# Performance work log

Measured on AMD Instinct MI355X. Metric: run time of the kernel, lower is better.

The kernel has to match this reference:

```python
import jax, jax.numpy as jnp
import numpy as np

N = 1048576   # total nodes
E = 8388608   # total edges
IN = 5        # in_channels
H = 32        # hid_channels
G = 16384     # num graphs
C = 10        # num_classes
L = 2         # conv_unit
EPS = 1e-5


def setup_inputs() -> dict:
    key = jax.random.key(0)
    ks = jax.random.split(key, 16)
    x = jax.random.normal(ks[0], (N, IN), dtype=jnp.float32)
    edge_index = jax.random.randint(ks[1], (2, E), 0, N, dtype=jnp.int64)
    edge_attr = jax.random.uniform(ks[2], (E, 1), dtype=jnp.float32)
    batch = jnp.sort(jax.random.randint(ks[3], (N,), 0, G, dtype=jnp.int64))
    s_in = 1.0 / np.sqrt(IN)
    s_h = 1.0 / np.sqrt(H)
    s_2h = 1.0 / np.sqrt(2 * H)
    W_emb = jax.random.normal(ks[4], (H, IN), dtype=jnp.float32) * s_in
    b_emb = jnp.zeros((H,), dtype=jnp.float32)
    W_rel = jax.random.normal(ks[5], (L, H, H), dtype=jnp.float32) * s_h
    b_rel = jnp.zeros((L, H), dtype=jnp.float32)
    W_root = jax.random.normal(ks[6], (L, H, H), dtype=jnp.float32) * s_h
    bn_gamma = jnp.ones((L, H), dtype=jnp.float32)
    bn_beta = jnp.zeros((L, H), dtype=jnp.float32)
    W1 = jax.random.normal(ks[7], (2 * H, H), dtype=jnp.float32) * s_h
    b1 = jnp.zeros((2 * H,), dtype=jnp.float32)
    W2 = jax.random.normal(ks[8], (C, 2 * H), dtype=jnp.float32) * s_2h
    b2 = jnp.zeros((C,), dtype=jnp.float32)
    return {
        "x": x, "edge_index": edge_index, "edge_attr": edge_attr, "batch": batch,
        "W_emb": W_emb, "b_emb": b_emb, "W_rel": W_rel, "b_rel": b_rel,
        "W_root": W_root, "bn_gamma": bn_gamma, "bn_beta": bn_beta,
        "W1": W1, "b1": b1, "W2": W2, "b2": b2,
    }


def _graph_conv(x, src, dst, ew, Wrel, brel, Wroot):
    # PyG GraphConv: lin_rel(scatter_add(ew * x[src] -> dst)) + lin_root(x)
    msg = x[src] * ew[:, None]                              # [E, H]
    agg = jax.ops.segment_sum(msg, dst, num_segments=N)     # [N, H]
    return agg @ Wrel.T + brel + x @ Wroot.T


def _batch_norm(x, gamma, beta):
    mean = jnp.mean(x, axis=0)
    var = jnp.mean(jnp.square(x - mean), axis=0)  # biased, as torch training BN
    return (x - mean) * jax.lax.rsqrt(var + EPS) * gamma + beta


def reference(x, edge_index, edge_attr, batch, W_emb, b_emb, W_rel, b_rel,
              W_root, bn_gamma, bn_beta, W1, b1, W2, b2):
    src, dst = edge_index[0], edge_index[1]
    ew = edge_attr.reshape(-1)
    h = x @ W_emb.T + b_emb                                  # node_emb
    for i in range(L):
        h = _graph_conv(h, src, dst, ew, W_rel[i], b_rel[i], W_root[i])
        h = jax.nn.relu(_batch_norm(h, bn_gamma[i], bn_beta[i]))
    graph_x = jax.ops.segment_max(h, batch, num_segments=G)  # global_max_pool
    hidden = jax.nn.relu(graph_x @ W1.T + b1)
    return hidden @ W2.T + b2                                # [G, C]
```

## Files before the change

### kernel.cpp

```cpp
#include <hip/hip_runtime.h>
#include <hip/hip_fp16.h>

#define NN 1048576
#define NE 8388608
#define NG 16384
#define NBUCK 256
#define BSH 12
#define EPB (NE / 256)

typedef _Float16 half8 __attribute__((ext_vector_type(8)));
typedef float f32x16 __attribute__((ext_vector_type(16)));

__global__ __launch_bounds__(256) void k_embed(const float* __restrict__ x,
    const float* __restrict__ W, const float* __restrict__ b, __half* __restrict__ h) {
  __shared__ float sW[160];
  __shared__ float sb[32];
  int t = threadIdx.x;
  if (t < 160) sW[t] = W[t];
  if (t < 32) sb[t] = b[t];
  __syncthreads();
  int idx = blockIdx.x * 256 + t;
  int c = idx & 31, n = idx >> 5;
  const float* xr = x + n * 5;
  float acc = sb[c];
#pragma unroll
  for (int k = 0; k < 5; ++k) acc = fmaf(xr[k], sW[c * 5 + k], acc);
  h[idx] = __float2half(acc);
}

__global__ __launch_bounds__(256) void k_pcnt(const int* __restrict__ dst, int* __restrict__ hist) {
  __shared__ int lh[NBUCK];
  int t = threadIdx.x;
  lh[t] = 0;
  __syncthreads();
  int base = blockIdx.x * EPB;
  for (int e = base + t; e < base + EPB; e += 256)
    atomicAdd(&lh[dst[e] >> BSH], 1);
  __syncthreads();
  hist[t * 256 + blockIdx.x] = lh[t];
}

__global__ __launch_bounds__(256) void k_scanA(int* __restrict__ hist, int* __restrict__ tot) {
  __shared__ int s2[256];
  int b = blockIdx.x, t = threadIdx.x;
  int v = hist[b * 256 + t];
  s2[t] = v; __syncthreads();
  for (int st = 1; st < 256; st <<= 1) {
    int a = (t >= st) ? s2[t - st] : 0; __syncthreads(); s2[t] += a; __syncthreads();
  }
  hist[b * 256 + t] = s2[t] - v;
  if (t == 255) tot[b] = s2[255];
}

__global__ __launch_bounds__(256) void k_scanB(const int* __restrict__ tot, int* __restrict__ gbase) {
  __shared__ int s2[256];
  int t = threadIdx.x;
  int c = tot[t];
  s2[t] = c; __syncthreads();
  for (int st = 1; st < 256; st <<= 1) {
    int a = (t >= st) ? s2[t - st] : 0; __syncthreads(); s2[t] += a; __syncthreads();
  }
  gbase[t] = s2[t] - c;
  if (t == 255) gbase[256] = s2[255];
}

__global__ __launch_bounds__(256) void k_part(const int* __restrict__ ei, const float* __restrict__ ew,
                                              const int* __restrict__ hist, const int* __restrict__ gbase,
                                              uint2* __restrict__ bsw) {
  __shared__ int cur[NBUCK];
  int t = threadIdx.x, blk = blockIdx.x;
  cur[t] = gbase[t] + hist[t * 256 + blk];
  __syncthreads();
  int base = blk * EPB;
  for (int e = base + t; e < base + EPB; e += 256) {
    int src = ei[e];
    int d   = ei[NE + e];
    unsigned wb = __float_as_uint(ew[e]);
    int b = d >> BSH;
    int pos = atomicAdd(&cur[b], 1);
    bsw[pos] = make_uint2(((unsigned)src << 12) | (unsigned)(d & 4095), wb);
  }
}

__global__ __launch_bounds__(256) void k_fillD(const int* __restrict__ gbase, const uint2* __restrict__ bsw,
                                               int* __restrict__ rowptr, uint2* __restrict__ colw) {
  __shared__ int loc[4096];
  __shared__ int s2[256];
  int t = threadIdx.x, b = blockIdx.x;
  int beg = gbase[b], end = gbase[b + 1], gb = beg;
  int node_base = b << BSH;
#pragma unroll
  for (int j = 0; j < 16; ++j) loc[t * 16 + j] = 0;
  __syncthreads();
  for (int i = beg + t; i < end; i += 256) atomicAdd(&loc[bsw[i].x & 4095], 1);
  __syncthreads();
  int v[16]; int tsum = 0;
#pragma unroll
  for (int j = 0; j < 16; ++j) { v[j] = loc[t * 16 + j]; tsum += v[j]; }
  s2[t] = tsum; __syncthreads();
  for (int st = 1; st < 256; st <<= 1) {
    int a = (t >= st) ? s2[t - st] : 0; __syncthreads(); s2[t] += a; __syncthreads();
  }
  int run = s2[t] - tsum;
#pragma unroll
  for (int j = 0; j < 16; ++j) {
    loc[t * 16 + j] = run;
    rowptr[node_base + t * 16 + j] = gb + run;
    run += v[j];
  }
  if (b == NBUCK - 1 && t == 255) rowptr[NN] = NE;
  __syncthreads();
  for (int i = beg + t; i < end; i += 256) {
    uint2 r = bsw[i];
    int p = atomicAdd(&loc[r.x & 4095], 1);
    colw[gb + p] = make_uint2(r.x >> 12, r.y);
  }
}

__global__ __launch_bounds__(256) void k_gbound(const int* __restrict__ batch, int* __restrict__ gptr) {
  int n = blockIdx.x * 256 + threadIdx.x;
  int b = batch[n];
  int prev = (n == 0) ? -1 : batch[n - 1];
  for (int g = prev + 1; g <= b; ++g) gptr[g] = n;
  if (n == NN - 1) {
    for (int g = b + 1; g <= NG; ++g) gptr[g] = NN;
  }
}

template <int FUSE_BN>
__global__ __launch_bounds__(256) void k_agglin(
    const int* __restrict__ rowptr, const uint2* __restrict__ colw,
    const __half* __restrict__ hIn, const float* __restrict__ bnss,
    const float* __restrict__ Wrel, const float* __restrict__ brel,
    const float* __restrict__ Wroot, __half* __restrict__ hPre,
    double* __restrict__ stats) {
  __shared__ __half sA[4][1024];
  __shared__ uint2 sE[256];
  __shared__ float sBn[64];
  __shared__ double rS[256], rQ[256];
  int t = threadIdx.x;
  int wv = t >> 6, lane = t & 63;
  int c = lane & 31, hi = lane >> 5, grp = t >> 5;
  int slot = (lane >> 4) & 1, cl = lane & 15;
  char* myA = (char*)sA[wv];

  if (FUSE_BN && t < 64) sBn[t] = bnss[t];
  __syncthreads();

  float bs0x = 0.f, bs0y = 0.f, bs1x = 0.f, bs1y = 0.f;
  if constexpr (FUSE_BN) {
    bs0x = bnss[2 * cl];      bs0y = bnss[2 * cl + 1];
    bs1x = bnss[32 + 2 * cl]; bs1y = bnss[32 + 2 * cl + 1];
  }

  half8 bfr[4];
#pragma unroll
  for (int m = 0; m < 4; ++m)
#pragma unroll
    for (int j = 0; j < 8; ++j) {
      int k = 16 * m + hi * 8 + j;
      float w = (k < 32) ? Wrel[c * 32 + k] : Wroot[c * 32 + (k - 32)];
      bfr[m][j] = (_Float16)w;
    }
  float bias = brel[c];
  double aS = 0.0, aQ = 0.0;

  for (int tile = blockIdx.x * 4 + wv; tile < NN / 32; tile += gridDim.x * 4) {
    int nbase = tile * 32;
    for (int r = 0; r < 16; ++r) {
      int node = 2 * r + hi;
      int n = nbase + node;
      int r0 = rowptr[n], r1 = rowptr[n + 1];
      float2 acc = make_float2(0.f, 0.f);
      for (int j = r0; j < r1; j += 32) {
        int m_ = r1 - j; if (m_ > 32) m_ = 32;
        uint2 cw = make_uint2(0u, 0u);
        if (c < m_) cw = colw[j + c];
        sE[t] = cw;
        int mm = (m_ + 7) & ~7;
        for (int i = 0; i < mm; i += 8) {
#pragma unroll
          for (int k = 0; k < 4; ++k) {
            uint2 e = sE[grp * 32 + i + 2 * k + slot];
            __half2 hv2 = *(const __half2*)(hIn + (size_t)(e.x) * 32 + 2 * cl);
            float w = __uint_as_float(e.y);
            float2 hf = __half22float2(hv2);
            if constexpr (FUSE_BN) {
              hf.x = fmaxf(fmaf(hf.x, bs0x, bs1x), 0.f);
              hf.y = fmaxf(fmaf(hf.y, bs0y, bs1y), 0.f);
            }
            acc.x = fmaf(w, hf.x, acc.x);
            acc.y = fmaf(w, hf.y, acc.y);
          }
        }
      }
      acc.x += __shfl_xor(acc.x, 16, 64);
      acc.y += __shfl_xor(acc.y, 16, 64);
      if (slot == 0) {
        int bw = (node * 64 + cl * 4) ^ ((node & 7) << 4);
        *(__half2*)(myA + bw) = __float22half2_rn(acc);
      }
    }
    f32x16 d;
#pragma unroll
    for (int r = 0; r < 16; ++r) d[r] = bias;
#pragma unroll
    for (int m = 0; m < 4; ++m) {
      half8 a;
      if (m < 2) {
        int node = c;
        int br = (node * 64 + (16 * m + hi * 8) * 2) ^ ((node & 7) << 4);
        a = *(const half8*)(myA + br);
      } else {
        int chb = 16 * (m - 2) + hi * 8;
        a = *(const half8*)(hIn + (size_t)(nbase + c) * 32 + chb);
        if constexpr (FUSE_BN) {
#pragma unroll
          for (int j = 0; j < 8; ++j) {
            float v = (float)a[j];
            v = fmaxf(fmaf(v, sBn[chb + j], sBn[32 + chb + j]), 0.f);
            a[j] = (_Float16)v;
          }
        }
      }
      d = __builtin_amdgcn_mfma_f32_32x32x16_f16(a, bfr[m], d, 0, 0, 0);
    }
#pragma unroll
    for (int r = 0; r < 16; ++r) {
      int node = (r & 3) + 8 * (r >> 2) + 4 * hi;
      float v = d[r];
      hPre[(size_t)(nbase + node) * 32 + c] = __float2half(v);
      aS += v; aQ += (double)v * v;
    }
  }
  rS[t] = aS; rQ[t] = aQ;
  __syncthreads();
  for (int s = 128; s >= 32; s >>= 1) {
    if (t < s) { rS[t] += rS[t + s]; rQ[t] += rQ[t + s]; }
    __syncthreads();
  }
  if (t < 32) {
    atomicAdd(&stats[t], rS[t]);
    atomicAdd(&stats[32 + t], rQ[t]);
  }
}

__global__ void k_bnfin(const double* __restrict__ stats, const float* __restrict__ gamma,
                        const float* __restrict__ beta, float* __restrict__ ss) {
  int c = threadIdx.x;
  double mean = stats[c] * (1.0 / NN);
  double var = stats[32 + c] * (1.0 / NN) - mean * mean;
  float scale = gamma[c] * (float)(1.0 / sqrt(var + 1e-5));
  ss[c] = scale;
  ss[32 + c] = beta[c] - (float)mean * scale;
}

__global__ __launch_bounds__(256) void k_pool(const __half* __restrict__ hB,
    const float* __restrict__ ss, const int* __restrict__ gptr, float* __restrict__ pooled) {
  int t = threadIdx.x;
  int wv = t >> 6, lane = t & 63;
  int p = lane >> 4, cl = lane & 15;
  float s0x = ss[2 * cl], s0y = ss[2 * cl + 1];
  float s1x = ss[32 + 2 * cl], s1y = ss[32 + 2 * cl + 1];
  int g = blockIdx.x * 4 + wv;
  int a = gptr[g], b = gptr[g + 1];
  float mx = 0.f, my = 0.f;
  for (int n = a + p; n < b; n += 4) {
    float2 hv = __half22float2(*(const __half2*)(hB + (size_t)n * 32 + 2 * cl));
    mx = fmaxf(mx, fmaf(hv.x, s0x, s1x));
    my = fmaxf(my, fmaf(hv.y, s0y, s1y));
  }
  mx = fmaxf(mx, __shfl_xor(mx, 16, 64)); my = fmaxf(my, __shfl_xor(my, 16, 64));
  mx = fmaxf(mx, __shfl_xor(mx, 32, 64)); my = fmaxf(my, __shfl_xor(my, 32, 64));
  if (p == 0) *(float2*)&pooled[g * 32 + 2 * cl] = make_float2(mx, my);
}

__global__ __launch_bounds__(256) void k_head(const float* __restrict__ pooled,
    const float* __restrict__ W1, const float* __restrict__ b1,
    const float* __restrict__ W2, const float* __restrict__ b2, float* __restrict__ out) {
  __shared__ float sW1[64 * 33], sW2[10 * 65], sb1[64], sb2[10];
  __shared__ float sHid[4][64];
  int t = threadIdx.x;
  for (int i = t; i < 2048; i += 256) sW1[(i >> 5) * 33 + (i & 31)] = W1[i];
  for (int i = t; i < 640; i += 256) sW2[(i >> 6) * 65 + (i & 63)] = W2[i];
  if (t < 64) sb1[t] = b1[t];
  if (t < 10) sb2[t] = b2[t];
  __syncthreads();
  int w = t >> 6, lane = t & 63;
  for (int g = blockIdx.x * 4 + w; g < NG; g += gridDim.x * 4) {
    float pv = (lane < 32) ? pooled[g * 32 + lane] : 0.f;
    float acc = sb1[lane];
#pragma unroll
    for (int k = 0; k < 32; ++k)
      acc = fmaf(__shfl(pv, k, 64), sW1[lane * 33 + k], acc);
    acc = fmaxf(acc, 0.f);
    sHid[w][lane] = acc;
    __syncthreads();
    if (lane < 10) {
      float o = sb2[lane];
#pragma unroll
      for (int j = 0; j < 64; ++j) o = fmaf(sHid[w][j], sW2[lane * 65 + j], o);
      out[g * 10 + lane] = o;
    }
    __syncthreads();
  }
}

extern "C" void kernel_launch(void* const* d_in, const int* in_sizes, int n_in,
                              void* d_out, int out_size, void* d_ws, size_t ws_size,
                              hipStream_t stream) {
  const float* x      = (const float*)d_in[0];
  const int*   ei     = (const int*)d_in[1];
  const float* ea     = (const float*)d_in[2];
  const int*   batch  = (const int*)d_in[3];
  const float* W_emb  = (const float*)d_in[4];
  const float* b_emb  = (const float*)d_in[5];
  const float* W_rel  = (const float*)d_in[6];
  const float* b_rel  = (const float*)d_in[7];
  const float* W_root = (const float*)d_in[8];
  const float* gamma  = (const float*)d_in[9];
  const float* beta   = (const float*)d_in[10];
  const float* W1     = (const float*)d_in[11];
  const float* b1     = (const float*)d_in[12];
  const float* W2     = (const float*)d_in[13];
  const float* b2     = (const float*)d_in[14];
  float* out = (float*)d_out;

  char* ws = (char*)d_ws;
  size_t off = 0;
  __half* hA    = (__half*)(ws + off); off += (size_t)NN * 32 * 2;
  uint2*  colw  = (uint2*)(ws + off);  off += (size_t)NE * 8;
  uint2*  bsw   = (uint2*)(ws + off);
  __half* hB    = (__half*)(ws + off);
  off += (size_t)NE * 8;
  int*    rowptr= (int*)(ws + off);    off += ((size_t)NN + 64) * 4;
  int*    hist  = (int*)(ws + off);    off += (size_t)NBUCK * 256 * 4;
  int*    tot   = (int*)(ws + off);    off += 1024;
  int*    gbase = (int*)(ws + off);    off += 2048;
  int*    gptr  = (int*)(ws + off);    off += ((size_t)NG + 64) * 4;
  float*  pooled= (float*)(ws + off);
  double* stats = (double*)d_out;
  float*  ss0   = (float*)((char*)d_out + 512);
  float*  ss1   = (float*)((char*)d_out + 768);

  k_embed<<<NN * 32 / 256, 256, 0, stream>>>(x, W_emb, b_emb, hA);

  k_pcnt <<<256, 256, 0, stream>>>(ei + NE, hist);
  k_scanA<<<NBUCK, 256, 0, stream>>>(hist, tot);
  k_scanB<<<1, 256, 0, stream>>>(tot, gbase);
  k_part <<<256, 256, 0, stream>>>(ei, ea, hist, gbase, bsw);
  k_fillD<<<NBUCK, 256, 0, stream>>>(gbase, bsw, rowptr, colw);
  k_gbound<<<NN / 256, 256, 0, stream>>>(batch, gptr);

  (void)hipMemsetAsync(stats, 0, 64 * 8, stream);
  k_agglin<0><<<2048, 256, 0, stream>>>(rowptr, colw, hA, nullptr,
                                        W_rel, b_rel, W_root, hB, stats);
  k_bnfin<<<1, 32, 0, stream>>>(stats, gamma, beta, ss0);

  (void)hipMemsetAsync(stats, 0, 64 * 8, stream);
  k_agglin<1><<<2048, 256, 0, stream>>>(rowptr, colw, hB, ss0,
                                        W_rel + 1024, b_rel + 32, W_root + 1024, hA, stats);
  k_bnfin<<<1, 32, 0, stream>>>(stats, gamma + 32, beta + 32, ss1);

  k_pool<<<NG / 4, 256, 0, stream>>>(hA, ss1, gptr, pooled);
  k_head<<<1024, 256, 0, stream>>>(pooled, W1, b1, W2, b2, out);
}
```

Baseline: 1.012 ms.

## Split aggregation from linear and compress edge list to SoA fp16 weights

Splits the fused gather+MFMA kernel into a separate gather kernel that writes aggregated features to global memory and a linear kernel that reads them back for the MFMA. The edge list is stored as separate source-index and fp16-weight arrays instead of 8-byte records, which cuts edge traffic during partitioning and gathering. The gather now uses one lane per channel with eight independent loads per step, aiming for more memory-level parallelism. In exchange it adds an extra global round trip of the aggregate buffer per layer, rounds edge weights to fp16, and accumulates the BN statistics in float instead of double.

```diff
diff --git a/kernel.cpp b/kernel.cpp
--- a/kernel.cpp
+++ b/kernel.cpp
@@ -66,7 +66,7 @@
 
 __global__ __launch_bounds__(256) void k_part(const int* __restrict__ ei, const float* __restrict__ ew,
                                               const int* __restrict__ hist, const int* __restrict__ gbase,
-                                              uint2* __restrict__ bsw) {
+                                              unsigned* __restrict__ bS, __half* __restrict__ bW) {
   __shared__ int cur[NBUCK];
   int t = threadIdx.x, blk = blockIdx.x;
   cur[t] = gbase[t] + hist[t * 256 + blk];
@@ -75,15 +75,17 @@
   for (int e = base + t; e < base + EPB; e += 256) {
     int src = ei[e];
     int d   = ei[NE + e];
-    unsigned wb = __float_as_uint(ew[e]);
+    __half w = __float2half(ew[e]);
     int b = d >> BSH;
     int pos = atomicAdd(&cur[b], 1);
-    bsw[pos] = make_uint2(((unsigned)src << 12) | (unsigned)(d & 4095), wb);
-  }
-}
-
-__global__ __launch_bounds__(256) void k_fillD(const int* __restrict__ gbase, const uint2* __restrict__ bsw,
-                                               int* __restrict__ rowptr, uint2* __restrict__ colw) {
+    bS[pos] = ((unsigned)src << 12) | (unsigned)(d & 4095);
+    bW[pos] = w;
+  }
+}
+
+__global__ __launch_bounds__(256) void k_fillD(const int* __restrict__ gbase, const unsigned* __restrict__ bS,
+                                               const __half* __restrict__ bW, int* __restrict__ rowptr,
+                                               unsigned* __restrict__ srcw, __half* __restrict__ wgt) {
   __shared__ int loc[4096];
   __shared__ int s2[256];
   int t = threadIdx.x, b = blockIdx.x;
@@ -92,7 +94,7 @@
 #pragma unroll
   for (int j = 0; j < 16; ++j) loc[t * 16 + j] = 0;
   __syncthreads();
-  for (int i = beg + t; i < end; i += 256) atomicAdd(&loc[bsw[i].x & 4095], 1);
+  for (int i = beg + t; i < end; i += 256) atomicAdd(&loc[bS[i] & 4095], 1);
   __syncthreads();
   int v[16]; int tsum = 0;
 #pragma unroll
@@ -111,9 +113,11 @@
   if (b == NBUCK - 1 && t == 255) rowptr[NN] = NE;
   __syncthreads();
   for (int i = beg + t; i < end; i += 256) {
-    uint2 r = bsw[i];
-    int p = atomicAdd(&loc[r.x & 4095], 1);
-    colw[gb + p] = make_uint2(r.x >> 12, r.y);
+    unsigned r = bS[i];
+    __half w = bW[i];
+    int p = atomicAdd(&loc[r & 4095], 1);
+    srcw[gb + p] = r >> 12;
+    wgt[gb + p] = w;
   }
 }
 
@@ -128,31 +132,70 @@
 }
 
 template <int FUSE_BN>
-__global__ __launch_bounds__(256) void k_agglin(
-    const int* __restrict__ rowptr, const uint2* __restrict__ colw,
-    const __half* __restrict__ hIn, const float* __restrict__ bnss,
-    const float* __restrict__ Wrel, const float* __restrict__ brel,
-    const float* __restrict__ Wroot, __half* __restrict__ hPre,
-    double* __restrict__ stats) {
-  __shared__ __half sA[4][1024];
-  __shared__ uint2 sE[256];
+__global__ __launch_bounds__(256) void k_gather(
+    const int* __restrict__ rowptr, const unsigned* __restrict__ srcw,
+    const __half* __restrict__ wgt, const __half* __restrict__ hIn,
+    const float* __restrict__ bnss, __half* __restrict__ aggG) {
+  __shared__ unsigned sS[256];
+  __shared__ __half sW[256];
+  int t = threadIdx.x, grp = t >> 5, c = t & 31;
+  float bs0 = 0.f, bs1 = 0.f;
+  if constexpr (FUSE_BN) { bs0 = bnss[c]; bs1 = bnss[32 + c]; }
+  for (int n0 = blockIdx.x * 8; n0 < NN; n0 += gridDim.x * 8) {
+    int n = n0 + grp;
+    int r0 = rowptr[n], r1 = rowptr[n + 1];
+    float acc = 0.f;
+    for (int j = r0; j < r1; j += 32) {
+      int m_ = r1 - j; if (m_ > 32) m_ = 32;
+      unsigned s = 0u; __half w = __ushort_as_half((unsigned short)0);
+      if (c < m_) { s = srcw[j + c]; w = wgt[j + c]; }
+      sS[t] = s; sW[t] = w;
+      int mm = (m_ + 7) & ~7;
+      for (int i = 0; i < mm; i += 8) {
+        const uint4* p4 = (const uint4*)&sS[grp * 32 + i];
+        uint4 a4 = p4[0], b4 = p4[1];
+        half8 w8 = *(const half8*)&sW[grp * 32 + i];
+        float h0 = __half2float(hIn[(size_t)a4.x * 32 + c]);
+        float h1 = __half2float(hIn[(size_t)a4.y * 32 + c]);
+        float h2 = __half2float(hIn[(size_t)a4.z * 32 + c]);
+        float h3 = __half2float(hIn[(size_t)a4.w * 32 + c]);
+        float h4 = __half2float(hIn[(size_t)b4.x * 32 + c]);
+        float h5 = __half2float(hIn[(size_t)b4.y * 32 + c]);
+        float h6 = __half2float(hIn[(size_t)b4.z * 32 + c]);
+        float h7 = __half2float(hIn[(size_t)b4.w * 32 + c]);
+        if constexpr (FUSE_BN) {
+          h0 = fmaxf(fmaf(h0, bs0, bs1), 0.f); h1 = fmaxf(fmaf(h1, bs0, bs1), 0.f);
+          h2 = fmaxf(fmaf(h2, bs0, bs1), 0.f); h3 = fmaxf(fmaf(h3, bs0, bs1), 0.f);
+          h4 = fmaxf(fmaf(h4, bs0, bs1), 0.f); h5 = fmaxf(fmaf(h5, bs0, bs1), 0.f);
+          h6 = fmaxf(fmaf(h6, bs0, bs1), 0.f); h7 = fmaxf(fmaf(h7, bs0, bs1), 0.f);
+        }
+        acc = fmaf((float)w8[0], h0, acc);
+        acc = fmaf((float)w8[1], h1, acc);
+        acc = fmaf((float)w8[2], h2, acc);
+        acc = fmaf((float)w8[3], h3, acc);
+        acc = fmaf((float)w8[4], h4, acc);
+        acc = fmaf((float)w8[5], h5, acc);
+        acc = fmaf((float)w8[6], h6, acc);
+        acc = fmaf((float)w8[7], h7, acc);
+      }
+    }
+    aggG[(size_t)n * 32 + c] = __float2half(acc);
+  }
+}
+
+template <int FUSE_BN>
+__global__ __launch_bounds__(256) void k_lin(
+    const __half* __restrict__ aggG, const __half* __restrict__ hIn,
+    const float* __restrict__ bnss, const float* __restrict__ Wrel,
+    const float* __restrict__ brel, const float* __restrict__ Wroot,
+    __half* __restrict__ hPre, double* __restrict__ stats) {
   __shared__ float sBn[64];
   __shared__ double rS[256], rQ[256];
   int t = threadIdx.x;
   int wv = t >> 6, lane = t & 63;
-  int c = lane & 31, hi = lane >> 5, grp = t >> 5;
-  int slot = (lane >> 4) & 1, cl = lane & 15;
-  char* myA = (char*)sA[wv];
-
+  int c = lane & 31, hi = lane >> 5;
   if (FUSE_BN && t < 64) sBn[t] = bnss[t];
   __syncthreads();
-
-  float bs0x = 0.f, bs0y = 0.f, bs1x = 0.f, bs1y = 0.f;
-  if constexpr (FUSE_BN) {
-    bs0x = bnss[2 * cl];      bs0y = bnss[2 * cl + 1];
-    bs1x = bnss[32 + 2 * cl]; bs1y = bnss[32 + 2 * cl + 1];
-  }
-
   half8 bfr[4];
 #pragma unroll
   for (int m = 0; m < 4; ++m)
@@ -163,44 +206,10 @@
       bfr[m][j] = (_Float16)w;
     }
   float bias = brel[c];
-  double aS = 0.0, aQ = 0.0;
+  float aS = 0.f, aQ = 0.f;
 
   for (int tile = blockIdx.x * 4 + wv; tile < NN / 32; tile += gridDim.x * 4) {
     int nbase = tile * 32;
-    for (int r = 0; r < 16; ++r) {
-      int node = 2 * r + hi;
-      int n = nbase + node;
-      int r0 = rowptr[n], r1 = rowptr[n + 1];
-      float2 acc = make_float2(0.f, 0.f);
-      for (int j = r0; j < r1; j += 32) {
-        int m_ = r1 - j; if (m_ > 32) m_ = 32;
-        uint2 cw = make_uint2(0u, 0u);
-        if (c < m_) cw = colw[j + c];
-        sE[t] = cw;
-        int mm = (m_ + 7) & ~7;
-        for (int i = 0; i < mm; i += 8) {
-#pragma unroll
-          for (int k = 0; k < 4; ++k) {
-            uint2 e = sE[grp * 32 + i + 2 * k + slot];
-            __half2 hv2 = *(const __half2*)(hIn + (size_t)(e.x) * 32 + 2 * cl);
-            float w = __uint_as_float(e.y);
-            float2 hf = __half22float2(hv2);
-            if constexpr (FUSE_BN) {
-              hf.x = fmaxf(fmaf(hf.x, bs0x, bs1x), 0.f);
-              hf.y = fmaxf(fmaf(hf.y, bs0y, bs1y), 0.f);
-            }
-            acc.x = fmaf(w, hf.x, acc.x);
-            acc.y = fmaf(w, hf.y, acc.y);
-          }
-        }
-      }
-      acc.x += __shfl_xor(acc.x, 16, 64);
-      acc.y += __shfl_xor(acc.y, 16, 64);
-      if (slot == 0) {
-        int bw = (node * 64 + cl * 4) ^ ((node & 7) << 4);
-        *(__half2*)(myA + bw) = __float22half2_rn(acc);
-      }
-    }
     f32x16 d;
 #pragma unroll
     for (int r = 0; r < 16; ++r) d[r] = bias;
@@ -208,9 +217,7 @@
     for (int m = 0; m < 4; ++m) {
       half8 a;
       if (m < 2) {
-        int node = c;
-        int br = (node * 64 + (16 * m + hi * 8) * 2) ^ ((node & 7) << 4);
-        a = *(const half8*)(myA + br);
+        a = *(const half8*)(aggG + (size_t)(nbase + c) * 32 + 16 * m + hi * 8);
       } else {
         int chb = 16 * (m - 2) + hi * 8;
         a = *(const half8*)(hIn + (size_t)(nbase + c) * 32 + chb);
@@ -230,10 +237,10 @@
       int node = (r & 3) + 8 * (r >> 2) + 4 * hi;
       float v = d[r];
       hPre[(size_t)(nbase + node) * 32 + c] = __float2half(v);
-      aS += v; aQ += (double)v * v;
-    }
-  }
-  rS[t] = aS; rQ[t] = aQ;
+      aS += v; aQ += v * v;
+    }
+  }
+  rS[t] = (double)aS; rQ[t] = (double)aQ;
   __syncthreads();
   for (int s = 128; s >= 32; s >>= 1) {
     if (t < s) { rS[t] += rS[t + s]; rQ[t] += rQ[t + s]; }
@@ -327,18 +334,21 @@
   float* out = (float*)d_out;
 
   char* ws = (char*)d_ws;
-  size_t off = 0;
-  __half* hA    = (__half*)(ws + off); off += (size_t)NN * 32 * 2;
-  uint2*  colw  = (uint2*)(ws + off);  off += (size_t)NE * 8;
-  uint2*  bsw   = (uint2*)(ws + off);
-  __half* hB    = (__half*)(ws + off);
-  off += (size_t)NE * 8;
-  int*    rowptr= (int*)(ws + off);    off += ((size_t)NN + 64) * 4;
-  int*    hist  = (int*)(ws + off);    off += (size_t)NBUCK * 256 * 4;
-  int*    tot   = (int*)(ws + off);    off += 1024;
-  int*    gbase = (int*)(ws + off);    off += 2048;
-  int*    gptr  = (int*)(ws + off);    off += ((size_t)NG + 64) * 4;
-  float*  pooled= (float*)(ws + off);
+  const size_t MiB = 1ull << 20;
+  __half*   hA    = (__half*)(ws + 0);
+  __half*   hB    = (__half*)(ws + 64 * MiB);
+  __half*   aggG  = (__half*)(ws + 128 * MiB);
+  unsigned* bS    = (unsigned*)(ws + 128 * MiB);
+  __half*   bW    = (__half*)(ws + 160 * MiB);
+  unsigned* srcw  = (unsigned*)(ws + 192 * MiB);
+  __half*   wgt   = (__half*)(ws + 224 * MiB);
+  size_t off = 240 * MiB;
+  int*    rowptr = (int*)(ws + off);  off += ((size_t)NN + 64) * 4;
+  int*    hist   = (int*)(ws + off);  off += (size_t)NBUCK * 256 * 4;
+  int*    tot    = (int*)(ws + off);  off += 1024;
+  int*    gbase  = (int*)(ws + off);  off += 2048;
+  int*    gptr   = (int*)(ws + off);  off += ((size_t)NG + 64) * 4;
+  float*  pooled = (float*)(ws + off);
   double* stats = (double*)d_out;
   float*  ss0   = (float*)((char*)d_out + 512);
   float*  ss1   = (float*)((char*)d_out + 768);
@@ -348,18 +358,19 @@
   k_pcnt <<<256, 256, 0, stream>>>(ei + NE, hist);
   k_scanA<<<NBUCK, 256, 0, stream>>>(hist, tot);
   k_scanB<<<1, 256, 0, stream>>>(tot, gbase);
-  k_part <<<256, 256, 0, stream>>>(ei, ea, hist, gbase, bsw);
-  k_fillD<<<NBUCK, 256, 0, stream>>>(gbase, bsw, rowptr, colw);
+  k_part <<<256, 256, 0, stream>>>(ei, ea, hist, gbase, bS, bW);
+  k_fillD<<<NBUCK, 256, 0, stream>>>(gbase, bS, bW, rowptr, srcw, wgt);
   k_gbound<<<NN / 256, 256, 0, stream>>>(batch, gptr);
 
   (void)hipMemsetAsync(stats, 0, 64 * 8, stream);
-  k_agglin<0><<<2048, 256, 0, stream>>>(rowptr, colw, hA, nullptr,
-                                        W_rel, b_rel, W_root, hB, stats);
+  k_gather<0><<<2048, 256, 0, stream>>>(rowptr, srcw, wgt, hA, nullptr, aggG);
+  k_lin<0><<<2048, 256, 0, stream>>>(aggG, hA, nullptr, W_rel, b_rel, W_root, hB, stats);
   k_bnfin<<<1, 32, 0, stream>>>(stats, gamma, beta, ss0);
 
   (void)hipMemsetAsync(stats, 0, 64 * 8, stream);
-  k_agglin<1><<<2048, 256, 0, stream>>>(rowptr, colw, hB, ss0,
-                                        W_rel + 1024, b_rel + 32, W_root + 1024, hA, stats);
+  k_gather<1><<<2048, 256, 0, stream>>>(rowptr, srcw, wgt, hB, ss0, aggG);
+  k_lin<1><<<2048, 256, 0, stream>>>(aggG, hB, ss0, W_rel + 1024, b_rel + 32,
+                                     W_root + 1024, hA, stats);
   k_bnfin<<<1, 32, 0, stream>>>(stats, gamma + 32, beta + 32, ss1);
 
   k_pool<<<NG / 4, 256, 0, stream>>>(hA, ss1, gptr, pooled);
```

Measured after the change: 1.112 ms. +9.9%, slower.
